# Optimization experiments

Measured on AMD Instinct MI355X. Metric: run time of the kernel, lower is better.

Reference implementation:

```python
import jax, jax.numpy as jnp
import numpy as np

N = 50000        # nodes
E = 1600000      # edges
G = 512          # graphs in batch
IN = 128         # in_dim
HID = 32         # hidden_dim
H = 4            # heads in conv1
NEG_SLOPE = 0.2  # PyG GATConv default


def setup_inputs() -> dict:
    key = jax.random.key(0)
    ks = jax.random.split(key, 20)
    s = 0.05
    return {
        "x": jax.random.normal(ks[0], (N, IN), jnp.float32),
        "edge_index": jax.random.randint(ks[1], (2, E), 0, N, dtype=jnp.int64),
        "edge_attr": jax.random.normal(ks[2], (E, 8), jnp.float32),
        "batch": jnp.sort(jax.random.randint(ks[3], (N,), 0, G, dtype=jnp.int64)),
        # conv1: in=IN, out=HID, heads=H, concat=True
        "W1": jax.random.normal(ks[4], (IN, H * HID), jnp.float32) * s,
        "a_src1": jax.random.normal(ks[5], (H, HID), jnp.float32) * s,
        "a_dst1": jax.random.normal(ks[6], (H, HID), jnp.float32) * s,
        "b1": jnp.zeros((H * HID,), jnp.float32),
        # conv2: in=H*HID, out=HID, heads=1, concat=False
        "W2": jax.random.normal(ks[7], (H * HID, HID), jnp.float32) * s,
        "a_src2": jax.random.normal(ks[8], (1, HID), jnp.float32) * s,
        "a_dst2": jax.random.normal(ks[9], (1, HID), jnp.float32) * s,
        "b2": jnp.zeros((HID,), jnp.float32),
        # classifier: HID -> HID//2 -> 1
        "Wc1": jax.random.normal(ks[10], (HID, HID // 2), jnp.float32) * s,
        "bc1": jnp.zeros((HID // 2,), jnp.float32),
        "Wc2": jax.random.normal(ks[11], (HID // 2, 1), jnp.float32) * s,
        "bc2": jnp.zeros((1,), jnp.float32),
    }


def gat_layer(x, src, dst, W, a_src, a_dst, b, heads, ch, concat, n):
    """PyG GATConv (eval mode): linear, edge-gathered additive attention,
    per-destination segment softmax, scatter-add aggregation."""
    h = (x @ W).reshape(n, heads, ch)                       # [N,H,C]
    alpha_s = jnp.sum(h * a_src, axis=-1)                   # [N,H]
    alpha_d = jnp.sum(h * a_dst, axis=-1)                   # [N,H]
    e = jax.nn.leaky_relu(alpha_s[src] + alpha_d[dst], NEG_SLOPE)  # [Etot,H]
    m = jax.lax.stop_gradient(jax.ops.segment_max(e, dst, num_segments=n))
    ex = jnp.exp(e - m[dst])
    den = jax.ops.segment_sum(ex, dst, num_segments=n)      # [N,H]
    alpha = ex / den[dst]                                   # [Etot,H]
    out = jax.ops.segment_sum(alpha[:, :, None] * h[src], dst, num_segments=n)
    out = out.reshape(n, heads * ch) if concat else out.mean(axis=1)
    return out + b


def reference(x, edge_index, edge_attr, batch,
              W1, a_src1, a_dst1, b1,
              W2, a_src2, a_dst2, b2,
              Wc1, bc1, Wc2, bc2):
    # add self-loops (PyG GATConv default)
    loop = jnp.arange(N, dtype=edge_index.dtype)
    src = jnp.concatenate([edge_index[0], loop])
    dst = jnp.concatenate([edge_index[1], loop])

    h = jax.nn.elu(gat_layer(x, src, dst, W1, a_src1, a_dst1, b1, H, HID, True, N))
    h = jax.nn.elu(gat_layer(h, src, dst, W2, a_src2, a_dst2, b2, 1, HID, False, N))

    # global mean pool over graphs
    cnt = jax.ops.segment_sum(jnp.ones((N,), h.dtype), batch, num_segments=G)
    pooled = jax.ops.segment_sum(h, batch, num_segments=G) / cnt[:, None]

    z = jax.nn.relu(pooled @ Wc1 + bc1)
    return (z @ Wc2 + bc2).squeeze(-1)   # [G]
```

## Files before the change

kernel.cpp:

```cpp
#include <hip/hip_runtime.h>
#include <math.h>

#define BUCKET_SHIFT 7
#define BUCKET_NODES (1 << BUCKET_SHIFT)
#define MAX_BUCK 512
#define PART_CHUNK 8192
#define PART_EPT 32

typedef _Float16 half4v __attribute__((ext_vector_type(4)));
typedef _Float16 half8v __attribute__((ext_vector_type(8)));

__device__ __forceinline__ float leaky02(float x){ return x > 0.f ? x : 0.2f * x; }
__device__ __forceinline__ float eluf(float x){ return x > 0.f ? x : expm1f(x); }

__global__ __launch_bounds__(128) void gemm1_kernel(
    const float* __restrict__ x, const float* __restrict__ W,
    const float* __restrict__ a_src, const float* __restrict__ a_dst,
    _Float16* __restrict__ h, float* __restrict__ as_, float* __restrict__ ad_, int n,
    int* __restrict__ zbase, int zwords)
{
  const int t = threadIdx.x;
  if (blockIdx.x == 0) {
    for (int i = t; i < zwords; i += 128) zbase[i] = 0;
  }
  const int row0 = blockIdx.x * 8;
  __shared__ float xs[8][128];
  __shared__ float sS[8][128];
  __shared__ float sD[8][128];
  for (int idx = t; idx < 8 * 32; idx += 128) {
    int r = idx >> 5, k4 = idx & 31;
    float4 v = (row0 + r < n) ? ((const float4*)x)[(size_t)(row0 + r) * 32 + k4]
                              : make_float4(0.f, 0.f, 0.f, 0.f);
    *(float4*)&xs[r][k4 * 4] = v;
  }
  __syncthreads();
  float acc[8] = {0,0,0,0,0,0,0,0};
  for (int k = 0; k < 128; k += 4) {
    float w0 = W[(k + 0) * 128 + t];
    float w1 = W[(k + 1) * 128 + t];
    float w2 = W[(k + 2) * 128 + t];
    float w3 = W[(k + 3) * 128 + t];
    #pragma unroll
    for (int r = 0; r < 8; ++r) {
      float4 xv = *(const float4*)&xs[r][k];
      acc[r] += xv.x * w0 + xv.y * w1 + xv.z * w2 + xv.w * w3;
    }
  }
  float asv = a_src[t], adv = a_dst[t];
  #pragma unroll
  for (int r = 0; r < 8; ++r) {
    float hv = acc[r];
    if (row0 + r < n) h[(size_t)(row0 + r) * 128 + t] = (_Float16)hv;
    sS[r][t] = hv * asv;
    sD[r][t] = hv * adv;
  }
  __syncthreads();
  if (t < 64) {
    int r = t >> 3, head = t & 3, which = (t >> 2) & 1;
    if (row0 + r < n) {
      const float (*buf)[128] = which ? sD : sS;
      double s = 0;
      for (int cc = 0; cc < 32; ++cc) s += (double)buf[r][head * 32 + cc];
      float* dstp = which ? ad_ : as_;
      dstp[(row0 + r) * 4 + head] = (float)s;
    }
  }
}

__global__ __launch_bounds__(128) void gemm2_kernel(
    const _Float16* __restrict__ x, const float* __restrict__ W,
    const float* __restrict__ a_src, const float* __restrict__ a_dst,
    _Float16* __restrict__ h, float* __restrict__ as_, float* __restrict__ ad_, int n)
{
  const int t = threadIdx.x;
  const int row0 = blockIdx.x * 8;
  __shared__ float xs[8][128];
  __shared__ float sH[8][32];
  for (int idx = t; idx < 8 * 16; idx += 128) {
    int r = idx >> 4, k8 = idx & 15;
    half8v v;
    #pragma unroll
    for (int q = 0; q < 8; ++q) v[q] = (_Float16)0.f;
    if (row0 + r < n) v = ((const half8v*)x)[(size_t)(row0 + r) * 16 + k8];
    #pragma unroll
    for (int q = 0; q < 8; ++q) xs[r][k8 * 8 + q] = (float)v[q];
  }
  __syncthreads();
  int col = t & 31, rp = t >> 5;
  int r0 = rp * 2, r1 = r0 + 1;
  float a0 = 0, a1 = 0;
  for (int k = 0; k < 128; k += 4) {
    float w0 = W[(k + 0) * 32 + col];
    float w1 = W[(k + 1) * 32 + col];
    float w2 = W[(k + 2) * 32 + col];
    float w3 = W[(k + 3) * 32 + col];
    float4 x0 = *(const float4*)&xs[r0][k];
    float4 x1 = *(const float4*)&xs[r1][k];
    a0 += x0.x * w0 + x0.y * w1 + x0.z * w2 + x0.w * w3;
    a1 += x1.x * w0 + x1.y * w1 + x1.z * w2 + x1.w * w3;
  }
  if (row0 + r0 < n) h[(size_t)(row0 + r0) * 32 + col] = (_Float16)a0;
  if (row0 + r1 < n) h[(size_t)(row0 + r1) * 32 + col] = (_Float16)a1;
  sH[r0][col] = a0; sH[r1][col] = a1;
  __syncthreads();
  if (t < 16) {
    int r = t >> 1, which = t & 1;
    if (row0 + r < n) {
      const float* a = which ? a_dst : a_src;
      double s = 0;
      for (int cc = 0; cc < 32; ++cc) s += (double)sH[r][cc] * (double)a[cc];
      (which ? ad_ : as_)[row0 + r] = (float)s;
    }
  }
}

__global__ __launch_bounds__(256) void bucket_hist_kernel(
    const int* __restrict__ dst, int* __restrict__ bucketCount, int E, int K)
{
  __shared__ int hist[MAX_BUCK];
  const int t = threadIdx.x;
  for (int b = t; b < K; b += 256) hist[b] = 0;
  __syncthreads();
  int cbase = blockIdx.x * PART_CHUNK;
  for (int j = 0; j < PART_EPT; ++j) {
    int e = cbase + j * 256 + t;
    if (e < E) atomicAdd(&hist[dst[e] >> BUCKET_SHIFT], 1);
  }
  __syncthreads();
  for (int b = t; b < K; b += 256)
    if (hist[b]) atomicAdd(&bucketCount[b], hist[b]);
}

__global__ __launch_bounds__(256) void scan_offsets_kernel(int* __restrict__ partial, int nb) {
  __shared__ int s[256];
  __shared__ int carry_s;
  int t = threadIdx.x;
  if (t == 0) carry_s = 0;
  __syncthreads();
  for (int b = 0; b < nb; b += 256) {
    int v = (b + t < nb) ? partial[b + t] : 0;
    s[t] = v;
    __syncthreads();
    for (int off = 1; off < 256; off <<= 1) {
      int x = (t >= off) ? s[t - off] : 0;
      __syncthreads();
      s[t] += x;
      __syncthreads();
    }
    int incl = s[t];
    int carry = carry_s;
    if (b + t < nb) partial[b + t] = carry + incl - v;
    __syncthreads();
    if (t == 255) carry_s = carry + incl;
    __syncthreads();
  }
}

__global__ __launch_bounds__(256) void partition_kernel(
    const int* __restrict__ src, const int* __restrict__ dst,
    const int* __restrict__ bucketStart, int* __restrict__ cursorB,
    unsigned int* __restrict__ bucketed, int E, int K)
{
  __shared__ int hist[MAX_BUCK];
  __shared__ int base_s[MAX_BUCK];
  __shared__ int cur[MAX_BUCK];
  for (int b = threadIdx.x; b < K; b += 256) hist[b] = 0;
  __syncthreads();
  int cbase = blockIdx.x * PART_CHUNK;
  for (int j = 0; j < PART_EPT; ++j) {
    int e = cbase + j * 256 + threadIdx.x;
    if (e < E) atomicAdd(&hist[dst[e] >> BUCKET_SHIFT], 1);
  }
  __syncthreads();
  for (int b = threadIdx.x; b < K; b += 256) {
    int c = hist[b];
    base_s[b] = c ? bucketStart[b] + atomicAdd(&cursorB[b], c) : 0;
    cur[b] = 0;
  }
  __syncthreads();
  for (int j = 0; j < PART_EPT; ++j) {
    int e = cbase + j * 256 + threadIdx.x;
    if (e < E) {
      int d = dst[e];
      int b = d >> BUCKET_SHIFT;
      int r = atomicAdd(&cur[b], 1);
      bucketed[base_s[b] + r] =
          ((unsigned int)src[e] << BUCKET_SHIFT) | (unsigned int)(d & (BUCKET_NODES - 1));
    }
  }
}

__global__ __launch_bounds__(256) void fill_csr_kernel(
    const unsigned int* __restrict__ bucketed, const int* __restrict__ bucketStart,
    int* __restrict__ rowStart, int* __restrict__ col, int n, int E, int K)
{
  int b = blockIdx.x;
  int nodeBase = b << BUCKET_SHIFT;
  int t = threadIdx.x;
  __shared__ int hist[BUCKET_NODES];
  __shared__ int rs[BUCKET_NODES];
  __shared__ int cur[BUCKET_NODES];
  if (t < BUCKET_NODES) hist[t] = 0;
  __syncthreads();
  int bs = bucketStart[b];
  int be = (b + 1 < K) ? bucketStart[b + 1] : E;
  for (int i = bs + t; i < be; i += 256)
    atomicAdd(&hist[bucketed[i] & (BUCKET_NODES - 1)], 1);
  __syncthreads();
  if (t < BUCKET_NODES) rs[t] = hist[t];
  __syncthreads();
  for (int off = 1; off < BUCKET_NODES; off <<= 1) {
    int v = (t < BUCKET_NODES && t >= off) ? rs[t - off] : 0;
    __syncthreads();
    if (t < BUCKET_NODES) rs[t] += v;
    __syncthreads();
  }
  if (t < BUCKET_NODES) {
    int node = nodeBase + t;
    int excl = bs + rs[t] - hist[t];
    if (node < n) rowStart[node] = excl;
    rs[t] = excl;
    cur[t] = 0;
  }
  if (b == K - 1 && t == 0) rowStart[n] = E;
  __syncthreads();
  for (int i = bs + t; i < be; i += 256) {
    unsigned int rec = bucketed[i];
    int local = rec & (BUCKET_NODES - 1);
    int pos = rs[local] + atomicAdd(&cur[local], 1);
    col[pos] = (int)(rec >> BUCKET_SHIFT);
  }
}

__global__ __launch_bounds__(256) void gat_aggr1_kernel(
    const _Float16* __restrict__ feat,
    const float* __restrict__ as_,
    const float* __restrict__ ad_,
    const int* __restrict__ rowStart,
    const int* __restrict__ col,
    const float* __restrict__ bias,
    _Float16* __restrict__ out, int n)
{
  constexpr int CHUNK = 16;
  const int t    = threadIdx.x;
  const int wave = t >> 6;
  const int lane = t & 63;
  const int grp  = lane >> 4;
  const int li   = lane & 15;
  const int slot = wave * 4 + grp;
  const int node = blockIdx.x * 16 + slot;
  const int hc   = li >> 2;

  __shared__ int   s_off[16][CHUNK];
  __shared__ float s_p[16][CHUNK * 4];

  if (node >= n) return;

  const int beg = rowStart[node];
  const int deg = rowStart[node + 1] - beg;

  const float4 advv = ((const float4*)ad_)[node];
  const float4 asvv = ((const float4*)as_)[node];
  const float adv[4] = {advv.x, advv.y, advv.z, advv.w};
  float es;
  {
    float e0 = leaky02(asvv.x + adv[0]);
    float e1 = leaky02(asvv.y + adv[1]);
    float e2 = leaky02(asvv.z + adv[2]);
    float e3 = leaky02(asvv.w + adv[3]);
    es = (hc == 0) ? e0 : (hc == 1) ? e1 : (hc == 2) ? e2 : e3;
  }
  const float ps = expf(es);

  const char* featc = (const char*)feat + (li << 4);
  const half8v fself = *(const half8v*)(featc + ((size_t)node << 8));
  double acc64[8];
  #pragma unroll
  for (int q = 0; q < 8; ++q) acc64[q] = (double)ps * (double)(float)fself[q];
  double den64 = (double)ps;

  int    st_s = 0;
  float4 st_q = make_float4(0.f, 0.f, 0.f, 0.f);
  if (deg > 0 && li < min(CHUNK, deg)) {
    st_s = col[beg + li];
    st_q = ((const float4*)as_)[st_s];
  }

  const int nch = (deg + CHUNK - 1) / CHUNK;
  for (int c = 0; c < nch; ++c) {
    const int base = c * CHUNK;
    const int cnt  = min(CHUNK, deg - base);
    if (li < cnt) {
      s_off[slot][li] = st_s << 8;
      float4 pp;
      pp.x = expf(leaky02(st_q.x + adv[0]));
      pp.y = expf(leaky02(st_q.y + adv[1]));
      pp.z = expf(leaky02(st_q.z + adv[2]));
      pp.w = expf(leaky02(st_q.w + adv[3]));
      *(float4*)&s_p[slot][li * 4] = pp;
    }
    __builtin_amdgcn_wave_barrier();
    const int nbase = base + CHUNK;
    if (nbase + li < deg) {
      st_s = col[beg + nbase + li];
      st_q = ((const float4*)as_)[st_s];
    }
    float a[8] = {0,0,0,0,0,0,0,0};
    float df = 0.f;
    if (cnt == CHUNK) {
      int off[16];
      #pragma unroll
      for (int j = 0; j < 16; ++j) off[j] = s_off[slot][j];
      half8v r[16];
      #pragma unroll
      for (int j = 0; j < 16; ++j) r[j] = *(const half8v*)(featc + off[j]);
      #pragma unroll
      for (int j = 0; j < 16; ++j) {
        float p = s_p[slot][j * 4 + hc];
        #pragma unroll
        for (int q = 0; q < 8; ++q) a[q] += p * (float)r[j][q];
        df += p;
      }
    } else {
      for (int j = 0; j < cnt; ++j) {
        int off = s_off[slot][j];
        float p = s_p[slot][j * 4 + hc];
        const half8v f = *(const half8v*)(featc + off);
        #pragma unroll
        for (int q = 0; q < 8; ++q) a[q] += p * (float)f[q];
        df += p;
      }
    }
    __builtin_amdgcn_wave_barrier();
    #pragma unroll
    for (int q = 0; q < 8; ++q) acc64[q] += a[q];
    den64 += df;
  }

  const float4 bv0 = ((const float4*)bias)[2 * li];
  const float4 bv1 = ((const float4*)bias)[2 * li + 1];
  const float bb[8] = {bv0.x, bv0.y, bv0.z, bv0.w, bv1.x, bv1.y, bv1.z, bv1.w};
  const double inv = 1.0 / den64;
  half8v ov;
  #pragma unroll
  for (int q = 0; q < 8; ++q)
    ov[q] = (_Float16)eluf((float)(acc64[q] * inv) + bb[q]);
  *(half8v*)((char*)out + ((size_t)node << 8) + (li << 4)) = ov;
}

__global__ __launch_bounds__(256) void gat_aggr2_kernel(
    const _Float16* __restrict__ feat,
    const float* __restrict__ as_,
    const float* __restrict__ ad_,
    const int* __restrict__ rowStart,
    const int* __restrict__ col,
    const float* __restrict__ bias,
    float* __restrict__ out, int n)
{
  constexpr int CHUNK = 16;
  const int t    = threadIdx.x;
  const int wave = t >> 6;
  const int lane = t & 63;
  const int grp  = lane >> 3;
  const int li   = lane & 7;
  const int slot = wave * 8 + grp;
  const int node = blockIdx.x * 32 + slot;

  __shared__ int   s_off[32][CHUNK];
  __shared__ float s_p[32][CHUNK];

  if (node >= n) return;

  const int beg = rowStart[node];
  const int deg = rowStart[node + 1] - beg;

  const float adv = ad_[node];
  const float ps  = expf(leaky02(as_[node] + adv));

  const char* featc = (const char*)feat + (li << 3);
  const half4v fself = *(const half4v*)(featc + ((size_t)node << 6));
  double acc64[4];
  acc64[0] = (double)ps * (double)(float)fself.x;
  acc64[1] = (double)ps * (double)(float)fself.y;
  acc64[2] = (double)ps * (double)(float)fself.z;
  acc64[3] = (double)ps * (double)(float)fself.w;
  double den64 = (double)ps;

  int   st_s0 = 0, st_s1 = 0;
  float st_q0 = 0.f, st_q1 = 0.f;
  if (deg > 0) {
    int c0 = min(CHUNK, deg);
    if (li < c0)     { st_s0 = col[beg + li];     st_q0 = as_[st_s0]; }
    if (li + 8 < c0) { st_s1 = col[beg + li + 8]; st_q1 = as_[st_s1]; }
  }

  const int nch = (deg + CHUNK - 1) / CHUNK;
  for (int c = 0; c < nch; ++c) {
    const int base = c * CHUNK;
    const int cnt  = min(CHUNK, deg - base);
    if (li < cnt)     { s_off[slot][li]     = st_s0 << 6; s_p[slot][li]     = expf(leaky02(st_q0 + adv)); }
    if (li + 8 < cnt) { s_off[slot][li + 8] = st_s1 << 6; s_p[slot][li + 8] = expf(leaky02(st_q1 + adv)); }
    __builtin_amdgcn_wave_barrier();
    const int nbase = base + CHUNK;
    if (nbase < deg) {
      if (nbase + li < deg)     { st_s0 = col[beg + nbase + li];     st_q0 = as_[st_s0]; }
      if (nbase + li + 8 < deg) { st_s1 = col[beg + nbase + li + 8]; st_q1 = as_[st_s1]; }
    }
    float a0 = 0.f, a1 = 0.f, a2 = 0.f, a3 = 0.f, df = 0.f;
    if (cnt == CHUNK) {
      int off[16];
      #pragma unroll
      for (int j = 0; j < 16; ++j) off[j] = s_off[slot][j];
      half4v r[16];
      #pragma unroll
      for (int j = 0; j < 16; ++j) r[j] = *(const half4v*)(featc + off[j]);
      #pragma unroll
      for (int j = 0; j < 16; ++j) {
        float p = s_p[slot][j];
        a0 += p * (float)r[j].x; a1 += p * (float)r[j].y;
        a2 += p * (float)r[j].z; a3 += p * (float)r[j].w;
        df += p;
      }
    } else {
      for (int j = 0; j < cnt; ++j) {
        int off = s_off[slot][j];
        float p = s_p[slot][j];
        const half4v f = *(const half4v*)(featc + off);
        a0 += p * (float)f.x; a1 += p * (float)f.y;
        a2 += p * (float)f.z; a3 += p * (float)f.w;
        df += p;
      }
    }
    __builtin_amdgcn_wave_barrier();
    acc64[0] += a0; acc64[1] += a1; acc64[2] += a2; acc64[3] += a3;
    den64 += df;
  }

  const double inv = 1.0 / den64;
  const float4 bv = *(const float4*)(bias + 4 * li);
  float4 o;
  o.x = eluf((float)(acc64[0] * inv) + bv.x);
  o.y = eluf((float)(acc64[1] * inv) + bv.y);
  o.z = eluf((float)(acc64[2] * inv) + bv.z);
  o.w = eluf((float)(acc64[3] * inv) + bv.w);
  *(float4*)(out + (size_t)node * 32 + 4 * li) = o;
}

__global__ __launch_bounds__(256) void pool_kernel(const float* __restrict__ act2,
    const int* __restrict__ batch, float* __restrict__ pooled,
    float* __restrict__ cnt, int n)
{
  int t = threadIdx.x;
  int c = t & 31, r = t >> 5;
  int n0 = blockIdx.x * 64 + r * 8;
  float run = 0.f; int gcur = -1; int len = 0;
  for (int i = 0; i < 8; ++i) {
    int nd = n0 + i;
    if (nd >= n) break;
    int gb = batch[nd];
    if (gb != gcur) {
      if (gcur >= 0) {
        atomicAdd(&pooled[gcur * 32 + c], run);
        if (c == 0) atomicAdd(&cnt[gcur], (float)len);
      }
      gcur = gb; run = 0.f; len = 0;
    }
    run += act2[(size_t)nd * 32 + c];
    len++;
  }
  if (gcur >= 0) {
    atomicAdd(&pooled[gcur * 32 + c], run);
    if (c == 0) atomicAdd(&cnt[gcur], (float)len);
  }
}

__global__ void classifier_kernel(const float* __restrict__ pooled, const float* __restrict__ cnt,
    const float* __restrict__ Wc1, const float* __restrict__ bc1,
    const float* __restrict__ Wc2, const float* __restrict__ bc2,
    float* __restrict__ outp, int g_total)
{
  int g = blockIdx.x * blockDim.x + threadIdx.x;
  if (g < g_total) {
    float inv = 1.0f / cnt[g];
    float pm[32];
    for (int c = 0; c < 32; ++c) pm[c] = pooled[g * 32 + c] * inv;
    double o = (double)bc2[0];
    for (int j = 0; j < 16; ++j) {
      double z = (double)bc1[j];
      for (int c = 0; c < 32; ++c) z += (double)pm[c] * (double)Wc1[c * 16 + j];
      float zr = (float)z;
      zr = zr > 0.f ? zr : 0.f;
      o += (double)zr * (double)Wc2[j];
    }
    outp[g] = (float)o;
  }
}

extern "C" void kernel_launch(void* const* d_in, const int* in_sizes, int n_in,
                              void* d_out, int out_size, void* d_ws, size_t ws_size,
                              hipStream_t stream)
{
  const float* x      = (const float*)d_in[0];
  const int*   ei     = (const int*)d_in[1];
  const int*   batch  = (const int*)d_in[3];
  const float* W1     = (const float*)d_in[4];
  const float* a_src1 = (const float*)d_in[5];
  const float* a_dst1 = (const float*)d_in[6];
  const float* b1     = (const float*)d_in[7];
  const float* W2     = (const float*)d_in[8];
  const float* a_src2 = (const float*)d_in[9];
  const float* a_dst2 = (const float*)d_in[10];
  const float* b2     = (const float*)d_in[11];
  const float* Wc1    = (const float*)d_in[12];
  const float* bc1    = (const float*)d_in[13];
  const float* Wc2    = (const float*)d_in[14];
  const float* bc2    = (const float*)d_in[15];

  const int N = in_sizes[0] / 128;
  const int E = in_sizes[1] / 2;
  const int G = out_size;

  const int* srcv = ei;
  const int* dstv = ei + E;

  char* ws = (char*)d_ws;
  size_t off = 0;
  auto alloc = [&](size_t bytes) -> void* {
    void* p = ws + off;
    off += (bytes + 255) & ~(size_t)255;
    return p;
  };
  _Float16* h1   = (_Float16*)alloc((size_t)N * 128 * 2);
  _Float16* act1 = (_Float16*)alloc((size_t)N * 128 * 2);
  _Float16* h2   = (_Float16*)alloc((size_t)N * 32 * 2);
  float* act2  = (float*)alloc((size_t)N * 32 * 4);
  float* as1   = (float*)alloc((size_t)N * 4 * 4);
  float* ad1   = (float*)alloc((size_t)N * 4 * 4);
  float* as2   = (float*)alloc((size_t)N * 4);
  float* ad2   = (float*)alloc((size_t)N * 4);
  int*   rowStart = (int*)alloc((size_t)(N + 1) * 4);
  int*   colv     = (int*)alloc((size_t)E * 4);
  unsigned int* bucketed = (unsigned int*)alloc((size_t)E * 4);
  size_t zoff0 = off;
  int*   bucketCount = (int*)alloc((size_t)MAX_BUCK * 4);
  int*   cursorB     = (int*)alloc((size_t)MAX_BUCK * 4);
  float* pooled      = (float*)alloc((size_t)G * 32 * 4);
  float* cntG        = (float*)alloc((size_t)G * 4);
  size_t zoff1 = off;
  const int zwords = (int)((zoff1 - zoff0) / 4);
  int* zbase = bucketCount;

  const int K = (N + BUCKET_NODES - 1) >> BUCKET_SHIFT;
  const int pb = (E + PART_CHUNK - 1) / PART_CHUNK;

  gemm1_kernel<<<(N + 7) / 8, 128, 0, stream>>>(x, W1, a_src1, a_dst1, h1, as1, ad1, N,
                                                zbase, zwords);
  bucket_hist_kernel<<<pb, 256, 0, stream>>>(dstv, bucketCount, E, K);
  scan_offsets_kernel<<<1, 256, 0, stream>>>(bucketCount, K);
  partition_kernel<<<pb, 256, 0, stream>>>(srcv, dstv, bucketCount, cursorB, bucketed, E, K);
  fill_csr_kernel<<<K, 256, 0, stream>>>(bucketed, bucketCount, rowStart, colv, N, E, K);

  gat_aggr1_kernel<<<(N + 15) / 16, 256, 0, stream>>>(h1, as1, ad1, rowStart, colv, b1, act1, N);

  gemm2_kernel<<<(N + 7) / 8, 128, 0, stream>>>(act1, W2, a_src2, a_dst2, h2, as2, ad2, N);
  gat_aggr2_kernel<<<(N + 31) / 32, 256, 0, stream>>>(h2, as2, ad2, rowStart, colv, b2, act2, N);

  pool_kernel<<<(N + 63) / 64, 256, 0, stream>>>(act2, batch, pooled, cntG, N);
  classifier_kernel<<<(G + 255) / 256, 256, 0, stream>>>(pooled, cntG, Wc1, bc1, Wc2, bc2,
                                                         (float*)d_out, G);
}
```

Measured before the change: 385.4 us.

## Fuse histogram into gemm1, use 2D scan partition, fp32 accumulators, fuse pooling

Merges the bucket histogram into the gemm1 launch as extra blocks that write per-chunk bucket counts. This enables a deterministic 2D scan and lets partition skip recomputing its histogram and the global cursor atomics. gemm1 now handles 16 rows per 256-thread block. Both aggregation kernels accumulate in float instead of double, and layer-2 aggregation atomically adds its outputs straight into the pooled sums, removing the act2 buffer and the pool kernel. The trade-offs are a serial per-bucket scan loop over about 200 chunks, many more pooling atomics per node, and reduced accumulation precision.

```diff
diff --git a/kernel.cpp b/kernel.cpp
--- a/kernel.cpp
+++ b/kernel.cpp
@@ -13,143 +13,107 @@
 __device__ __forceinline__ float leaky02(float x){ return x > 0.f ? x : 0.2f * x; }
 __device__ __forceinline__ float eluf(float x){ return x > 0.f ? x : expm1f(x); }
 
-__global__ __launch_bounds__(128) void gemm1_kernel(
+__global__ __launch_bounds__(256) void gemm1_hist_kernel(
     const float* __restrict__ x, const float* __restrict__ W,
     const float* __restrict__ a_src, const float* __restrict__ a_dst,
     _Float16* __restrict__ h, float* __restrict__ as_, float* __restrict__ ad_, int n,
+    const int* __restrict__ dstv, int* __restrict__ bucketPartial, int pbPad,
+    int E, int K, int histBlocks,
     int* __restrict__ zbase, int zwords)
 {
   const int t = threadIdx.x;
-  if (blockIdx.x == 0) {
-    for (int i = t; i < zwords; i += 128) zbase[i] = 0;
-  }
-  const int row0 = blockIdx.x * 8;
-  __shared__ float xs[8][128];
-  __shared__ float sS[8][128];
-  __shared__ float sD[8][128];
-  for (int idx = t; idx < 8 * 32; idx += 128) {
+  if (blockIdx.x < histBlocks) {
+    __shared__ int hist[MAX_BUCK];
+    for (int b = t; b < K; b += 256) hist[b] = 0;
+    __syncthreads();
+    const int j = blockIdx.x;
+    int cbase = j * PART_CHUNK;
+    for (int q = 0; q < PART_EPT; ++q) {
+      int e = cbase + q * 256 + t;
+      if (e < E) atomicAdd(&hist[dstv[e] >> BUCKET_SHIFT], 1);
+    }
+    __syncthreads();
+    for (int b = t; b < K; b += 256)
+      bucketPartial[(size_t)b * pbPad + j] = hist[b];
+    if (j == 0) {
+      for (int i = t; i < zwords; i += 256) zbase[i] = 0;
+    }
+    return;
+  }
+  const int g = blockIdx.x - histBlocks;
+  const int row0 = g * 16;
+  __shared__ float xs[16][128];
+  __shared__ float sS[16][128];
+  __shared__ float sD[16][128];
+  for (int idx = t; idx < 16 * 32; idx += 256) {
     int r = idx >> 5, k4 = idx & 31;
     float4 v = (row0 + r < n) ? ((const float4*)x)[(size_t)(row0 + r) * 32 + k4]
                               : make_float4(0.f, 0.f, 0.f, 0.f);
     *(float4*)&xs[r][k4 * 4] = v;
   }
   __syncthreads();
+  const int col = t & 127, hf = t >> 7;
   float acc[8] = {0,0,0,0,0,0,0,0};
   for (int k = 0; k < 128; k += 4) {
-    float w0 = W[(k + 0) * 128 + t];
-    float w1 = W[(k + 1) * 128 + t];
-    float w2 = W[(k + 2) * 128 + t];
-    float w3 = W[(k + 3) * 128 + t];
+    float w0 = W[(k + 0) * 128 + col];
+    float w1 = W[(k + 1) * 128 + col];
+    float w2 = W[(k + 2) * 128 + col];
+    float w3 = W[(k + 3) * 128 + col];
     #pragma unroll
     for (int r = 0; r < 8; ++r) {
-      float4 xv = *(const float4*)&xs[r][k];
+      const float4 xv = *(const float4*)&xs[hf * 8 + r][k];
       acc[r] += xv.x * w0 + xv.y * w1 + xv.z * w2 + xv.w * w3;
     }
   }
-  float asv = a_src[t], adv = a_dst[t];
+  float asv = a_src[col], adv = a_dst[col];
   #pragma unroll
   for (int r = 0; r < 8; ++r) {
+    int row = hf * 8 + r;
     float hv = acc[r];
-    if (row0 + r < n) h[(size_t)(row0 + r) * 128 + t] = (_Float16)hv;
-    sS[r][t] = hv * asv;
-    sD[r][t] = hv * adv;
-  }
-  __syncthreads();
-  if (t < 64) {
-    int r = t >> 3, head = t & 3, which = (t >> 2) & 1;
+    if (row0 + row < n) h[(size_t)(row0 + row) * 128 + col] = (_Float16)hv;
+    sS[row][col] = hv * asv;
+    sD[row][col] = hv * adv;
+  }
+  __syncthreads();
+  if (t < 128) {
+    int r = t >> 3, head = (t >> 1) & 3, which = t & 1;
     if (row0 + r < n) {
       const float (*buf)[128] = which ? sD : sS;
-      double s = 0;
-      for (int cc = 0; cc < 32; ++cc) s += (double)buf[r][head * 32 + cc];
-      float* dstp = which ? ad_ : as_;
-      dstp[(row0 + r) * 4 + head] = (float)s;
-    }
-  }
-}
-
-__global__ __launch_bounds__(128) void gemm2_kernel(
-    const _Float16* __restrict__ x, const float* __restrict__ W,
-    const float* __restrict__ a_src, const float* __restrict__ a_dst,
-    _Float16* __restrict__ h, float* __restrict__ as_, float* __restrict__ ad_, int n)
-{
-  const int t = threadIdx.x;
-  const int row0 = blockIdx.x * 8;
-  __shared__ float xs[8][128];
-  __shared__ float sH[8][32];
-  for (int idx = t; idx < 8 * 16; idx += 128) {
-    int r = idx >> 4, k8 = idx & 15;
-    half8v v;
-    #pragma unroll
-    for (int q = 0; q < 8; ++q) v[q] = (_Float16)0.f;
-    if (row0 + r < n) v = ((const half8v*)x)[(size_t)(row0 + r) * 16 + k8];
-    #pragma unroll
-    for (int q = 0; q < 8; ++q) xs[r][k8 * 8 + q] = (float)v[q];
-  }
-  __syncthreads();
-  int col = t & 31, rp = t >> 5;
-  int r0 = rp * 2, r1 = r0 + 1;
-  float a0 = 0, a1 = 0;
-  for (int k = 0; k < 128; k += 4) {
-    float w0 = W[(k + 0) * 32 + col];
-    float w1 = W[(k + 1) * 32 + col];
-    float w2 = W[(k + 2) * 32 + col];
-    float w3 = W[(k + 3) * 32 + col];
-    float4 x0 = *(const float4*)&xs[r0][k];
-    float4 x1 = *(const float4*)&xs[r1][k];
-    a0 += x0.x * w0 + x0.y * w1 + x0.z * w2 + x0.w * w3;
-    a1 += x1.x * w0 + x1.y * w1 + x1.z * w2 + x1.w * w3;
-  }
-  if (row0 + r0 < n) h[(size_t)(row0 + r0) * 32 + col] = (_Float16)a0;
-  if (row0 + r1 < n) h[(size_t)(row0 + r1) * 32 + col] = (_Float16)a1;
-  sH[r0][col] = a0; sH[r1][col] = a1;
-  __syncthreads();
-  if (t < 16) {
-    int r = t >> 1, which = t & 1;
-    if (row0 + r < n) {
-      const float* a = which ? a_dst : a_src;
-      double s = 0;
-      for (int cc = 0; cc < 32; ++cc) s += (double)sH[r][cc] * (double)a[cc];
-      (which ? ad_ : as_)[row0 + r] = (float)s;
-    }
-  }
-}
-
-__global__ __launch_bounds__(256) void bucket_hist_kernel(
-    const int* __restrict__ dst, int* __restrict__ bucketCount, int E, int K)
-{
-  __shared__ int hist[MAX_BUCK];
-  const int t = threadIdx.x;
-  for (int b = t; b < K; b += 256) hist[b] = 0;
-  __syncthreads();
-  int cbase = blockIdx.x * PART_CHUNK;
-  for (int j = 0; j < PART_EPT; ++j) {
-    int e = cbase + j * 256 + t;
-    if (e < E) atomicAdd(&hist[dst[e] >> BUCKET_SHIFT], 1);
-  }
-  __syncthreads();
-  for (int b = t; b < K; b += 256)
-    if (hist[b]) atomicAdd(&bucketCount[b], hist[b]);
-}
-
-__global__ __launch_bounds__(256) void scan_offsets_kernel(int* __restrict__ partial, int nb) {
+      double s2 = 0;
+      for (int cc = 0; cc < 32; ++cc) s2 += (double)buf[r][head * 32 + cc];
+      (which ? ad_ : as_)[(row0 + r) * 4 + head] = (float)s2;
+    }
+  }
+}
+
+__global__ __launch_bounds__(256) void scan2d_kernel(
+    int* __restrict__ partial, int pbPad, int* __restrict__ bucketStart, int pb, int K)
+{
+  int t = threadIdx.x;
+  for (int b = t; b < K; b += 256) {
+    int run = 0;
+    int* row = partial + (size_t)b * pbPad;
+    for (int j = 0; j < pb; ++j) { int v = row[j]; row[j] = run; run += v; }
+    bucketStart[b] = run;
+  }
+  __syncthreads();
   __shared__ int s[256];
   __shared__ int carry_s;
-  int t = threadIdx.x;
   if (t == 0) carry_s = 0;
   __syncthreads();
-  for (int b = 0; b < nb; b += 256) {
-    int v = (b + t < nb) ? partial[b + t] : 0;
+  for (int base = 0; base < K; base += 256) {
+    int v = (base + t < K) ? bucketStart[base + t] : 0;
     s[t] = v;
     __syncthreads();
     for (int off = 1; off < 256; off <<= 1) {
-      int x = (t >= off) ? s[t - off] : 0;
+      int xv = (t >= off) ? s[t - off] : 0;
       __syncthreads();
-      s[t] += x;
+      s[t] += xv;
       __syncthreads();
     }
     int incl = s[t];
     int carry = carry_s;
-    if (b + t < nb) partial[b + t] = carry + incl - v;
+    if (base + t < K) bucketStart[base + t] = carry + incl - v;
     __syncthreads();
     if (t == 255) carry_s = carry + incl;
     __syncthreads();
@@ -158,28 +122,20 @@
 
 __global__ __launch_bounds__(256) void partition_kernel(
     const int* __restrict__ src, const int* __restrict__ dst,
-    const int* __restrict__ bucketStart, int* __restrict__ cursorB,
+    const int* __restrict__ bucketStart, const int* __restrict__ pre, int pbPad,
     unsigned int* __restrict__ bucketed, int E, int K)
 {
-  __shared__ int hist[MAX_BUCK];
   __shared__ int base_s[MAX_BUCK];
   __shared__ int cur[MAX_BUCK];
-  for (int b = threadIdx.x; b < K; b += 256) hist[b] = 0;
-  __syncthreads();
-  int cbase = blockIdx.x * PART_CHUNK;
-  for (int j = 0; j < PART_EPT; ++j) {
-    int e = cbase + j * 256 + threadIdx.x;
-    if (e < E) atomicAdd(&hist[dst[e] >> BUCKET_SHIFT], 1);
-  }
-  __syncthreads();
+  const int j = blockIdx.x;
   for (int b = threadIdx.x; b < K; b += 256) {
-    int c = hist[b];
-    base_s[b] = c ? bucketStart[b] + atomicAdd(&cursorB[b], c) : 0;
+    base_s[b] = bucketStart[b] + pre[(size_t)b * pbPad + j];
     cur[b] = 0;
   }
   __syncthreads();
-  for (int j = 0; j < PART_EPT; ++j) {
-    int e = cbase + j * 256 + threadIdx.x;
+  int cbase = j * PART_CHUNK;
+  for (int q = 0; q < PART_EPT; ++q) {
+    int e = cbase + q * 256 + threadIdx.x;
     if (e < E) {
       int d = dst[e];
       int b = d >> BUCKET_SHIFT;
@@ -274,10 +230,10 @@
 
   const char* featc = (const char*)feat + (li << 4);
   const half8v fself = *(const half8v*)(featc + ((size_t)node << 8));
-  double acc64[8];
+  float accf[8];
   #pragma unroll
-  for (int q = 0; q < 8; ++q) acc64[q] = (double)ps * (double)(float)fself[q];
-  double den64 = (double)ps;
+  for (int q = 0; q < 8; ++q) accf[q] = ps * (float)fself[q];
+  float den = ps;
 
   int    st_s = 0;
   float4 st_q = make_float4(0.f, 0.f, 0.f, 0.f);
@@ -333,29 +289,77 @@
     }
     __builtin_amdgcn_wave_barrier();
     #pragma unroll
-    for (int q = 0; q < 8; ++q) acc64[q] += a[q];
-    den64 += df;
+    for (int q = 0; q < 8; ++q) accf[q] += a[q];
+    den += df;
   }
 
   const float4 bv0 = ((const float4*)bias)[2 * li];
   const float4 bv1 = ((const float4*)bias)[2 * li + 1];
   const float bb[8] = {bv0.x, bv0.y, bv0.z, bv0.w, bv1.x, bv1.y, bv1.z, bv1.w};
-  const double inv = 1.0 / den64;
+  const float inv = 1.0f / den;
   half8v ov;
   #pragma unroll
   for (int q = 0; q < 8; ++q)
-    ov[q] = (_Float16)eluf((float)(acc64[q] * inv) + bb[q]);
+    ov[q] = (_Float16)eluf(accf[q] * inv + bb[q]);
   *(half8v*)((char*)out + ((size_t)node << 8) + (li << 4)) = ov;
 }
 
-__global__ __launch_bounds__(256) void gat_aggr2_kernel(
+__global__ __launch_bounds__(128) void gemm2_kernel(
+    const _Float16* __restrict__ x, const float* __restrict__ W,
+    const float* __restrict__ a_src, const float* __restrict__ a_dst,
+    _Float16* __restrict__ h, float* __restrict__ as_, float* __restrict__ ad_, int n)
+{
+  const int t = threadIdx.x;
+  const int row0 = blockIdx.x * 8;
+  __shared__ float xs[8][128];
+  __shared__ float sH[8][32];
+  for (int idx = t; idx < 8 * 16; idx += 128) {
+    int r = idx >> 4, k8 = idx & 15;
+    half8v v;
+    #pragma unroll
+    for (int q = 0; q < 8; ++q) v[q] = (_Float16)0.f;
+    if (row0 + r < n) v = ((const half8v*)x)[(size_t)(row0 + r) * 16 + k8];
+    #pragma unroll
+    for (int q = 0; q < 8; ++q) xs[r][k8 * 8 + q] = (float)v[q];
+  }
+  __syncthreads();
+  int col = t & 31, rp = t >> 5;
+  int r0 = rp * 2, r1 = r0 + 1;
+  float a0 = 0, a1 = 0;
+  for (int k = 0; k < 128; k += 4) {
+    float w0 = W[(k + 0) * 32 + col];
+    float w1 = W[(k + 1) * 32 + col];
+    float w2 = W[(k + 2) * 32 + col];
+    float w3 = W[(k + 3) * 32 + col];
+    float4 x0 = *(const float4*)&xs[r0][k];
+    float4 x1 = *(const float4*)&xs[r1][k];
+    a0 += x0.x * w0 + x0.y * w1 + x0.z * w2 + x0.w * w3;
+    a1 += x1.x * w0 + x1.y * w1 + x1.z * w2 + x1.w * w3;
+  }
+  if (row0 + r0 < n) h[(size_t)(row0 + r0) * 32 + col] = (_Float16)a0;
+  if (row0 + r1 < n) h[(size_t)(row0 + r1) * 32 + col] = (_Float16)a1;
+  sH[r0][col] = a0; sH[r1][col] = a1;
+  __syncthreads();
+  if (t < 16) {
+    int r = t >> 1, which = t & 1;
+    if (row0 + r < n) {
+      const float* a = which ? a_dst : a_src;
+      double s = 0;
+      for (int cc = 0; cc < 32; ++cc) s += (double)sH[r][cc] * (double)a[cc];
+      (which ? ad_ : as_)[row0 + r] = (float)s;
+    }
+  }
+}
+
+__global__ __launch_bounds__(256) void gat_aggr2_pool_kernel(
     const _Float16* __restrict__ feat,
     const float* __restrict__ as_,
     const float* __restrict__ ad_,
     const int* __restrict__ rowStart,
     const int* __restrict__ col,
     const float* __restrict__ bias,
-    float* __restrict__ out, int n)
+    const int* __restrict__ batch,
+    float* __restrict__ pooled, float* __restrict__ cntG, int n)
 {
   constexpr int CHUNK = 16;
   const int t    = threadIdx.x;
@@ -379,12 +383,11 @@
 
   const char* featc = (const char*)feat + (li << 3);
   const half4v fself = *(const half4v*)(featc + ((size_t)node << 6));
-  double acc64[4];
-  acc64[0] = (double)ps * (double)(float)fself.x;
-  acc64[1] = (double)ps * (double)(float)fself.y;
-  acc64[2] = (double)ps * (double)(float)fself.z;
-  acc64[3] = (double)ps * (double)(float)fself.w;
-  double den64 = (double)ps;
+  float a0s = ps * (float)fself.x;
+  float a1s = ps * (float)fself.y;
+  float a2s = ps * (float)fself.z;
+  float a3s = ps * (float)fself.w;
+  float den = ps;
 
   int   st_s0 = 0, st_s1 = 0;
   float st_q0 = 0.f, st_q1 = 0.f;
@@ -432,46 +435,23 @@
       }
     }
     __builtin_amdgcn_wave_barrier();
-    acc64[0] += a0; acc64[1] += a1; acc64[2] += a2; acc64[3] += a3;
-    den64 += df;
-  }
-
-  const double inv = 1.0 / den64;
+    a0s += a0; a1s += a1; a2s += a2; a3s += a3;
+    den += df;
+  }
+
+  const float inv = 1.0f / den;
   const float4 bv = *(const float4*)(bias + 4 * li);
-  float4 o;
-  o.x = eluf((float)(acc64[0] * inv) + bv.x);
-  o.y = eluf((float)(acc64[1] * inv) + bv.y);
-  o.z = eluf((float)(acc64[2] * inv) + bv.z);
-  o.w = eluf((float)(acc64[3] * inv) + bv.w);
-  *(float4*)(out + (size_t)node * 32 + 4 * li) = o;
-}
-
-__global__ __launch_bounds__(256) void pool_kernel(const float* __restrict__ act2,
-    const int* __restrict__ batch, float* __restrict__ pooled,
-    float* __restrict__ cnt, int n)
-{
-  int t = threadIdx.x;
-  int c = t & 31, r = t >> 5;
-  int n0 = blockIdx.x * 64 + r * 8;
-  float run = 0.f; int gcur = -1; int len = 0;
-  for (int i = 0; i < 8; ++i) {
-    int nd = n0 + i;
-    if (nd >= n) break;
-    int gb = batch[nd];
-    if (gb != gcur) {
-      if (gcur >= 0) {
-        atomicAdd(&pooled[gcur * 32 + c], run);
-        if (c == 0) atomicAdd(&cnt[gcur], (float)len);
-      }
-      gcur = gb; run = 0.f; len = 0;
-    }
-    run += act2[(size_t)nd * 32 + c];
-    len++;
-  }
-  if (gcur >= 0) {
-    atomicAdd(&pooled[gcur * 32 + c], run);
-    if (c == 0) atomicAdd(&cnt[gcur], (float)len);
-  }
+  float o0 = eluf(a0s * inv + bv.x);
+  float o1 = eluf(a1s * inv + bv.y);
+  float o2 = eluf(a2s * inv + bv.z);
+  float o3 = eluf(a3s * inv + bv.w);
+  const int g = batch[node];
+  float* pp = pooled + (size_t)g * 32 + 4 * li;
+  atomicAdd(pp + 0, o0);
+  atomicAdd(pp + 1, o1);
+  atomicAdd(pp + 2, o2);
+  atomicAdd(pp + 3, o3);
+  if (li == 0) atomicAdd(&cntG[g], 1.0f);
 }
 
 __global__ void classifier_kernel(const float* __restrict__ pooled, const float* __restrict__ cnt,
@@ -530,10 +510,13 @@
     off += (bytes + 255) & ~(size_t)255;
     return p;
   };
+  const int K  = (N + BUCKET_NODES - 1) >> BUCKET_SHIFT;
+  const int pb = (E + PART_CHUNK - 1) / PART_CHUNK;
+  const int pbPad = (pb + 63) & ~63;
+
   _Float16* h1   = (_Float16*)alloc((size_t)N * 128 * 2);
   _Float16* act1 = (_Float16*)alloc((size_t)N * 128 * 2);
   _Float16* h2   = (_Float16*)alloc((size_t)N * 32 * 2);
-  float* act2  = (float*)alloc((size_t)N * 32 * 4);
   float* as1   = (float*)alloc((size_t)N * 4 * 4);
   float* ad1   = (float*)alloc((size_t)N * 4 * 4);
   float* as2   = (float*)alloc((size_t)N * 4);
@@ -541,31 +524,27 @@
   int*   rowStart = (int*)alloc((size_t)(N + 1) * 4);
   int*   colv     = (int*)alloc((size_t)E * 4);
   unsigned int* bucketed = (unsigned int*)alloc((size_t)E * 4);
+  int*   bucketPartial = (int*)alloc((size_t)MAX_BUCK * pbPad * 4);
+  int*   bucketStart   = (int*)alloc((size_t)MAX_BUCK * 4);
   size_t zoff0 = off;
-  int*   bucketCount = (int*)alloc((size_t)MAX_BUCK * 4);
-  int*   cursorB     = (int*)alloc((size_t)MAX_BUCK * 4);
-  float* pooled      = (float*)alloc((size_t)G * 32 * 4);
-  float* cntG        = (float*)alloc((size_t)G * 4);
+  float* pooled = (float*)alloc((size_t)G * 32 * 4);
+  float* cntG   = (float*)alloc((size_t)G * 4);
   size_t zoff1 = off;
   const int zwords = (int)((zoff1 - zoff0) / 4);
-  int* zbase = bucketCount;
-
-  const int K = (N + BUCKET_NODES - 1) >> BUCKET_SHIFT;
-  const int pb = (E + PART_CHUNK - 1) / PART_CHUNK;
-
-  gemm1_kernel<<<(N + 7) / 8, 128, 0, stream>>>(x, W1, a_src1, a_dst1, h1, as1, ad1, N,
-                                                zbase, zwords);
-  bucket_hist_kernel<<<pb, 256, 0, stream>>>(dstv, bucketCount, E, K);
-  scan_offsets_kernel<<<1, 256, 0, stream>>>(bucketCount, K);
-  partition_kernel<<<pb, 256, 0, stream>>>(srcv, dstv, bucketCount, cursorB, bucketed, E, K);
-  fill_csr_kernel<<<K, 256, 0, stream>>>(bucketed, bucketCount, rowStart, colv, N, E, K);
-
+  int* zbase = (int*)pooled;
+
+  const int gemmBlocks = (N + 15) / 16;
+  gemm1_hist_kernel<<<pb + gemmBlocks, 256, 0, stream>>>(
+      x, W1, a_src1, a_dst1, h1, as1, ad1, N,
+      dstv, bucketPartial, pbPad, E, K, pb, zbase, zwords);
+  scan2d_kernel<<<1, 256, 0, stream>>>(bucketPartial, pbPad, bucketStart, pb, K);
+  partition_kernel<<<pb, 256, 0, stream>>>(srcv, dstv, bucketStart, bucketPartial, pbPad,
+                                           bucketed, E, K);
+  fill_csr_kernel<<<K, 256, 0, stream>>>(bucketed, bucketStart, rowStart, colv, N, E, K);
   gat_aggr1_kernel<<<(N + 15) / 16, 256, 0, stream>>>(h1, as1, ad1, rowStart, colv, b1, act1, N);
-
   gemm2_kernel<<<(N + 7) / 8, 128, 0, stream>>>(act1, W2, a_src2, a_dst2, h2, as2, ad2, N);
-  gat_aggr2_kernel<<<(N + 31) / 32, 256, 0, stream>>>(h2, as2, ad2, rowStart, colv, b2, act2, N);
-
-  pool_kernel<<<(N + 63) / 64, 256, 0, stream>>>(act2, batch, pooled, cntG, N);
+  gat_aggr2_pool_kernel<<<(N + 31) / 32, 256, 0, stream>>>(h2, as2, ad2, rowStart, colv, b2,
+                                                           batch, pooled, cntG, N);
   classifier_kernel<<<(G + 255) / 256, 256, 0, stream>>>(pooled, cntG, Wc1, bc1, Wc2, bc2,
                                                          (float*)d_out, G);
 }
```

Result: slower. 527.6 us (+36.9%).
